# Kernel optimization log

Hardware: AMD Instinct MI355X
Metric: run time of the kernel (lower is better)

Reference implementation:

```python
import jax, jax.numpy as jnp
import numpy as np

HEADS = 8
DIM_HEAD = 64


def setup_inputs() -> dict:
    key = jax.random.key(0)
    ks = jax.random.split(key, 9)
    b, n, d = 2, 2048, 512
    inner = HEADS * DIM_HEAD  # 512
    s = 0.02
    return {
        "x": jax.random.normal(ks[0], (b, n, d), dtype=jnp.float32),
        "attn_bias": jax.random.normal(ks[1], (1, HEADS, n, n), dtype=jnp.float32),
        "Wq": jax.random.normal(ks[2], (d, inner), dtype=jnp.float32) * s,
        "Wkv": jax.random.normal(ks[3], (d, 2 * inner), dtype=jnp.float32) * s,
        "Wo": jax.random.normal(ks[4], (inner, d), dtype=jnp.float32) * s,
        "bo": jax.random.normal(ks[5], (d,), dtype=jnp.float32) * s,
        "Wg": jax.random.normal(ks[6], (d, inner), dtype=jnp.float32) * s,
        "bg": jnp.ones((inner,), dtype=jnp.float32),
    }


def reference(x, attn_bias, Wq, Wkv, Wo, bo, Wg, bg):
    b, n, d = x.shape
    h, dh = HEADS, DIM_HEAD
    scale = dh ** -0.5
    # projections: [b, n, h*dh] -> [b, h, n, dh]
    q = (x @ Wq).reshape(b, n, h, dh).transpose(0, 2, 1, 3) * scale
    k, v = jnp.split(x @ Wkv, 2, axis=-1)
    k = k.reshape(b, n, h, dh).transpose(0, 2, 1, 3)
    v = v.reshape(b, n, h, dh).transpose(0, 2, 1, 3)
    # scores + additive bias; max-subtract softmax (stable, as in original)
    dots = jnp.einsum('bhid,bhjd->bhij', q, k) + attn_bias
    attn = jax.nn.softmax(dots, axis=-1)
    out = jnp.einsum('bhij,bhjd->bhid', attn, v)
    out = out.transpose(0, 2, 1, 3).reshape(b, n, h * dh)
    # gating sigmoid epilogue
    gates = jax.nn.sigmoid(x @ Wg + bg)
    out = out * gates
    return out @ Wo + bo
```

## Files before the change

### kernel.cpp

```cpp
#include <hip/hip_runtime.h>
#include <hip/hip_bf16.h>

typedef __bf16 bf16_t;
typedef __bf16 bf16x8 __attribute__((ext_vector_type(8)));
typedef float f32x4 __attribute__((ext_vector_type(4)));

static __device__ __forceinline__ bf16_t to_bf16(float f) { return (bf16_t)f; }

__global__ void k_convert_x(const float* __restrict__ src, bf16_t* __restrict__ dst, int n8) {
  int i = blockIdx.x * blockDim.x + threadIdx.x;
  if (i >= n8) return;
  const float4* s = reinterpret_cast<const float4*>(src) + (size_t)i * 2;
  float4 a = s[0], b = s[1];
  bf16x8 v;
  v[0]=(bf16_t)a.x; v[1]=(bf16_t)a.y; v[2]=(bf16_t)a.z; v[3]=(bf16_t)a.w;
  v[4]=(bf16_t)b.x; v[5]=(bf16_t)b.y; v[6]=(bf16_t)b.z; v[7]=(bf16_t)b.w;
  reinterpret_cast<bf16x8*>(dst)[i] = v;
}

__global__ void k_transpose_cvt(const float* __restrict__ src, bf16_t* __restrict__ dst, int Nc) {
  __shared__ bf16_t tile[64 * 72];
  const int n0 = blockIdx.x * 64, k0 = blockIdx.y * 64;
  const int t = threadIdx.x;
  #pragma unroll
  for (int it = 0; it < 16; ++it) {
    int c = t + it * 256;
    int kl = c >> 6, nl = c & 63;
    tile[kl * 72 + nl] = to_bf16(src[(size_t)(k0 + kl) * Nc + n0 + nl]);
  }
  __syncthreads();
  #pragma unroll
  for (int it = 0; it < 16; ++it) {
    int c = t + it * 256;
    int nl = c >> 6, kl = c & 63;
    dst[(size_t)(n0 + nl) * 512 + k0 + kl] = tile[kl * 72 + nl];
  }
}

__global__ __launch_bounds__(256) void k_gemm_proj(
    const bf16_t* __restrict__ A,
    const bf16_t* __restrict__ BT,
    const float*  __restrict__ bg,
    bf16_t* __restrict__ qo,
    bf16_t* __restrict__ ko,
    bf16_t* __restrict__ vto,
    float*  __restrict__ go)
{
  __shared__ __align__(16) bf16_t lA[128 * 72];
  __shared__ __align__(16) bf16_t lB[128 * 72];
  const int t = threadIdx.x;
  const int w = t >> 6, lane = t & 63, lr = lane & 15, lg = lane >> 4;
  const int wr = w >> 1, wc = w & 1;
  const int m0 = blockIdx.y * 128, n0 = blockIdx.x * 128;
  f32x4 acc[4][4] = {};
  for (int k0 = 0; k0 < 512; k0 += 64) {
    __syncthreads();
    #pragma unroll
    for (int it = 0; it < 4; ++it) {
      int c = t + it * 256;
      int row = c >> 3, cc = c & 7;
      *reinterpret_cast<bf16x8*>(&lA[row * 72 + cc * 8]) =
          *reinterpret_cast<const bf16x8*>(&A[(size_t)(m0 + row) * 512 + k0 + cc * 8]);
      *reinterpret_cast<bf16x8*>(&lB[row * 72 + cc * 8]) =
          *reinterpret_cast<const bf16x8*>(&BT[(size_t)(n0 + row) * 512 + k0 + cc * 8]);
    }
    __syncthreads();
    #pragma unroll
    for (int kk = 0; kk < 2; ++kk) {
      bf16x8 af[4], bfm[4];
      #pragma unroll
      for (int mf = 0; mf < 4; ++mf)
        af[mf] = *reinterpret_cast<const bf16x8*>(&lA[(wr*64 + mf*16 + lr) * 72 + kk*32 + lg*8]);
      #pragma unroll
      for (int nf = 0; nf < 4; ++nf)
        bfm[nf] = *reinterpret_cast<const bf16x8*>(&lB[(wc*64 + nf*16 + lr) * 72 + kk*32 + lg*8]);
      #pragma unroll
      for (int mf = 0; mf < 4; ++mf)
        #pragma unroll
        for (int nf = 0; nf < 4; ++nf)
          acc[mf][nf] = __builtin_amdgcn_mfma_f32_16x16x32_bf16(af[mf], bfm[nf], acc[mf][nf], 0, 0, 0);
    }
  }
  const int seg = n0 >> 9;
  #pragma unroll
  for (int mf = 0; mf < 4; ++mf) {
    #pragma unroll
    for (int nf = 0; nf < 4; ++nf) {
      #pragma unroll
      for (int r = 0; r < 4; ++r) {
        int rm = m0 + wr*64 + mf*16 + lg*4 + r;
        int cn = n0 + wc*64 + nf*16 + lr;
        float v = acc[mf][nf][r];
        int b = rm >> 11, n = rm & 2047;
        int c = cn & 511;
        if (seg == 0) {
          int h = c >> 6, dh = c & 63;
          qo[((size_t)(b*8 + h) * 2048 + n) * 64 + dh] = to_bf16(v * 0.125f);
        } else if (seg == 1) {
          int h = c >> 6, dh = c & 63;
          ko[((size_t)(b*8 + h) * 2048 + n) * 64 + dh] = to_bf16(v);
        } else if (seg == 2) {
          int h = c >> 6, dh = c & 63;
          vto[((size_t)(b*8 + h) * 64 + dh) * 2048 + n] = to_bf16(v);
        } else {
          float z = v + bg[c];
          go[(size_t)rm * 512 + c] = 1.0f / (1.0f + __expf(-z));
        }
      }
    }
  }
}

#define M_FIX 8.0f
template<int FINAL>
__global__ __launch_bounds__(256, 4) void k_attn(
    const bf16_t* __restrict__ q,
    const bf16_t* __restrict__ kb,
    const bf16_t* __restrict__ vt,
    const float*  __restrict__ bias,
    const float*  __restrict__ gates,
    bf16_t* __restrict__ ao,
    float* __restrict__ pO,
    float* __restrict__ pl)
{
  __shared__ __align__(16) bf16_t lK[64 * 72];
  __shared__ __align__(16) bf16_t lV[64 * 72];
  __shared__ __align__(16) bf16_t lP[4][16 * 72];
  const int t = threadIdx.x, w = t >> 6, lane = t & 63, lr = lane & 15, lg = lane >> 4;
  const int bh = blockIdx.y, b = bh >> 3, h = bh & 7;
  const int i0 = blockIdx.x * 64, ib = i0 + w * 16;
  const int ntile = 32 / (int)gridDim.z;
  const int sz = blockIdx.z;
  const int jbase = sz * ntile * 64;

  bf16x8 aq[2];
  const bf16_t* qp = q + ((size_t)bh * 2048 + ib + lr) * 64;
  aq[0] = *reinterpret_cast<const bf16x8*>(qp + lg * 8);
  aq[1] = *reinterpret_cast<const bf16x8*>(qp + 32 + lg * 8);

  float l_r[4] = {0.f, 0.f, 0.f, 0.f};
  f32x4 accO[4] = {};

  const float* bias_p = bias + (size_t)h * 2048 * 2048 + (size_t)(ib + lg * 4) * 2048 + lr;
  const bf16_t* kp = kb + (size_t)bh * 2048 * 64;
  const bf16_t* vp = vt + (size_t)bh * 64 * 2048;

  const int srow = t >> 3, scc = t & 7;
  const int srow1 = (t + 256) >> 3;

  bf16x8 rK0, rK1, rV0, rV1;
  float bv[4][4];
  {
    const int j0 = jbase;
    rK0 = *reinterpret_cast<const bf16x8*>(&kp[(size_t)(j0 + srow)  * 64 + scc * 8]);
    rK1 = *reinterpret_cast<const bf16x8*>(&kp[(size_t)(j0 + srow1) * 64 + scc * 8]);
    rV0 = *reinterpret_cast<const bf16x8*>(&vp[(size_t)srow  * 2048 + j0 + scc * 8]);
    rV1 = *reinterpret_cast<const bf16x8*>(&vp[(size_t)srow1 * 2048 + j0 + scc * 8]);
    #pragma unroll
    for (int nf = 0; nf < 4; ++nf)
      #pragma unroll
      for (int r = 0; r < 4; ++r)
        bv[nf][r] = bias_p[(size_t)r * 2048 + j0 + nf * 16];
  }

  for (int jt = 0; jt < ntile; ++jt) {
    const int j1 = jbase + (jt + 1) * 64;
    const bool more = (jt + 1 < ntile);

    __syncthreads();
    *reinterpret_cast<bf16x8*>(&lK[srow  * 72 + scc * 8]) = rK0;
    *reinterpret_cast<bf16x8*>(&lK[srow1 * 72 + scc * 8]) = rK1;
    *reinterpret_cast<bf16x8*>(&lV[srow  * 72 + scc * 8]) = rV0;
    *reinterpret_cast<bf16x8*>(&lV[srow1 * 72 + scc * 8]) = rV1;
    __syncthreads();

    if (more) {
      rK0 = *reinterpret_cast<const bf16x8*>(&kp[(size_t)(j1 + srow)  * 64 + scc * 8]);
      rK1 = *reinterpret_cast<const bf16x8*>(&kp[(size_t)(j1 + srow1) * 64 + scc * 8]);
      rV0 = *reinterpret_cast<const bf16x8*>(&vp[(size_t)srow  * 2048 + j1 + scc * 8]);
      rV1 = *reinterpret_cast<const bf16x8*>(&vp[(size_t)srow1 * 2048 + j1 + scc * 8]);
    }

    f32x4 s[4] = {};
    #pragma unroll
    for (int kk = 0; kk < 2; ++kk) {
      #pragma unroll
      for (int nf = 0; nf < 4; ++nf) {
        bf16x8 bf = *reinterpret_cast<const bf16x8*>(&lK[(nf*16 + lr) * 72 + kk*32 + lg*8]);
        s[nf] = __builtin_amdgcn_mfma_f32_16x16x32_bf16(aq[kk], bf, s[nf], 0, 0, 0);
      }
    }
    #pragma unroll
    for (int nf = 0; nf < 4; ++nf) {
      #pragma unroll
      for (int r = 0; r < 4; ++r) {
        float p = __expf(s[nf][r] + bv[nf][r] - M_FIX);
        s[nf][r] = p;
        l_r[r] += p;
        lP[w][(lg*4 + r) * 72 + nf*16 + lr] = to_bf16(p);
      }
    }
    if (more) {
      #pragma unroll
      for (int nf = 0; nf < 4; ++nf)
        #pragma unroll
        for (int r = 0; r < 4; ++r)
          bv[nf][r] = bias_p[(size_t)r * 2048 + j1 + nf * 16];
    }

    #pragma unroll
    for (int kk = 0; kk < 2; ++kk) {
      bf16x8 pa = *reinterpret_cast<const bf16x8*>(&lP[w][lr * 72 + kk*32 + lg*8]);
      #pragma unroll
      for (int df = 0; df < 4; ++df) {
        bf16x8 bv8 = *reinterpret_cast<const bf16x8*>(&lV[(df*16 + lr) * 72 + kk*32 + lg*8]);
        accO[df] = __builtin_amdgcn_mfma_f32_16x16x32_bf16(pa, bv8, accO[df], 0, 0, 0);
      }
    }
  }

  #pragma unroll
  for (int r = 0; r < 4; ++r) {
    float rs = l_r[r];
    rs += __shfl_xor(rs, 1); rs += __shfl_xor(rs, 2);
    rs += __shfl_xor(rs, 4); rs += __shfl_xor(rs, 8);
    l_r[r] = rs;
  }

  if (FINAL) {
    #pragma unroll
    for (int r = 0; r < 4; ++r) {
      float inv = 1.0f / l_r[r];
      int ig = ib + lg*4 + r;
      #pragma unroll
      for (int df = 0; df < 4; ++df) {
        int dg = h*64 + df*16 + lr;
        float gate = gates[(size_t)(b*2048 + ig) * 512 + dg];
        ao[(size_t)(b*2048 + ig) * 512 + dg] = to_bf16(accO[df][r] * inv * gate);
      }
    }
  } else {
    float* po = pO + (((size_t)sz * 16 + bh) * 2048) * 64;
    #pragma unroll
    for (int r = 0; r < 4; ++r) {
      int ig = ib + lg*4 + r;
      #pragma unroll
      for (int df = 0; df < 4; ++df)
        po[(size_t)ig * 64 + df*16 + lr] = accO[df][r];
    }
    if (lr == 0) {
      size_t rb = ((size_t)sz * 16 + bh) * 2048 + ib + lg*4;
      #pragma unroll
      for (int r = 0; r < 4; ++r) pl[rb + r] = l_r[r];
    }
  }
}

__global__ __launch_bounds__(256) void k_attn_combine(
    const float* __restrict__ pO, const float* __restrict__ pl,
    const float* __restrict__ gates, bf16_t* __restrict__ ao, int nsplit)
{
  int idx = blockIdx.x * 256 + threadIdx.x;
  int dh = idx & 63, row = (idx >> 6) & 2047, bh = idx >> 17;
  int b = bh >> 3, h = bh & 7;
  const size_t SP_O = (size_t)16 * 2048 * 64, SP_S = (size_t)16 * 2048;
  size_t rb = (size_t)bh * 2048 + row;
  float L = 0.f, O = 0.f;
  for (int s = 0; s < nsplit; ++s) {
    L += pl[s * SP_S + rb];
    O += pO[s * SP_O + rb * 64 + dh];
  }
  float gate = gates[(size_t)(b * 2048 + row) * 512 + h * 64 + dh];
  ao[(size_t)(b * 2048 + row) * 512 + h * 64 + dh] = to_bf16(O / L * gate);
}

__global__ __launch_bounds__(256) void k_gemm_out(
    const bf16_t* __restrict__ A,
    const bf16_t* __restrict__ BT,
    const float*  __restrict__ bo,
    float* __restrict__ out)
{
  __shared__ __align__(16) bf16_t lA[128 * 72];
  __shared__ __align__(16) bf16_t lB[128 * 72];
  const int t = threadIdx.x;
  const int w = t >> 6, lane = t & 63, lr = lane & 15, lg = lane >> 4;
  const int wr = w >> 1, wc = w & 1;
  const int m0 = blockIdx.y * 128, n0 = blockIdx.x * 128;
  f32x4 acc[4][4] = {};
  for (int k0 = 0; k0 < 512; k0 += 64) {
    __syncthreads();
    #pragma unroll
    for (int it = 0; it < 4; ++it) {
      int c = t + it * 256;
      int row = c >> 3, cc = c & 7;
      *reinterpret_cast<bf16x8*>(&lA[row * 72 + cc * 8]) =
          *reinterpret_cast<const bf16x8*>(&A[(size_t)(m0 + row) * 512 + k0 + cc * 8]);
      *reinterpret_cast<bf16x8*>(&lB[row * 72 + cc * 8]) =
          *reinterpret_cast<const bf16x8*>(&BT[(size_t)(n0 + row) * 512 + k0 + cc * 8]);
    }
    __syncthreads();
    #pragma unroll
    for (int kk = 0; kk < 2; ++kk) {
      bf16x8 af[4], bfm[4];
      #pragma unroll
      for (int mf = 0; mf < 4; ++mf)
        af[mf] = *reinterpret_cast<const bf16x8*>(&lA[(wr*64 + mf*16 + lr) * 72 + kk*32 + lg*8]);
      #pragma unroll
      for (int nf = 0; nf < 4; ++nf)
        bfm[nf] = *reinterpret_cast<const bf16x8*>(&lB[(wc*64 + nf*16 + lr) * 72 + kk*32 + lg*8]);
      #pragma unroll
      for (int mf = 0; mf < 4; ++mf)
        #pragma unroll
        for (int nf = 0; nf < 4; ++nf)
          acc[mf][nf] = __builtin_amdgcn_mfma_f32_16x16x32_bf16(af[mf], bfm[nf], acc[mf][nf], 0, 0, 0);
    }
  }
  #pragma unroll
  for (int mf = 0; mf < 4; ++mf) {
    #pragma unroll
    for (int nf = 0; nf < 4; ++nf) {
      #pragma unroll
      for (int r = 0; r < 4; ++r) {
        int rm = m0 + wr*64 + mf*16 + lg*4 + r;
        int cn = n0 + wc*64 + nf*16 + lr;
        out[(size_t)rm * 512 + cn] = acc[mf][nf][r] + bo[cn];
      }
    }
  }
}

extern "C" void kernel_launch(void* const* d_in, const int* in_sizes, int n_in,
                              void* d_out, int out_size, void* d_ws, size_t ws_size,
                              hipStream_t stream) {
  const float* x    = (const float*)d_in[0];
  const float* bias = (const float*)d_in[1];
  const float* Wq   = (const float*)d_in[2];
  const float* Wkv  = (const float*)d_in[3];
  const float* Wo   = (const float*)d_in[4];
  const float* bo   = (const float*)d_in[5];
  const float* Wg   = (const float*)d_in[6];
  const float* bg   = (const float*)d_in[7];
  float* out = (float*)d_out;

  char* ws = (char*)d_ws;
  const size_t MB = 1024 * 1024;
  bf16_t* x_bf  = (bf16_t*)(ws + 0 * MB);
  bf16_t* WcatT = (bf16_t*)(ws + 4 * MB);
  bf16_t* WoT   = (bf16_t*)(ws + 6 * MB);
  bf16_t* q_bf  = (bf16_t*)(ws + 7 * MB);
  bf16_t* k_bf  = (bf16_t*)(ws + 11 * MB);
  bf16_t* vt_bf = (bf16_t*)(ws + 15 * MB);
  float*  g_f32 = (float*) (ws + 19 * MB);
  bf16_t* ao_bf = (bf16_t*)(ws + 27 * MB);

  int NS = (ws_size >= 66 * MB) ? 4 : (ws_size >= 48 * MB ? 2 : 1);
  float* pO = (float*)(ws + 31 * MB);
  float* pl = (float*)(ws + 31 * MB + (size_t)NS * 8 * MB);

  k_convert_x<<<1024, 256, 0, stream>>>(x, x_bf, 2097152 / 8);
  k_transpose_cvt<<<dim3(8, 8),  256, 0, stream>>>(Wq,  WcatT,               512);
  k_transpose_cvt<<<dim3(16, 8), 256, 0, stream>>>(Wkv, WcatT + 512 * 512,  1024);
  k_transpose_cvt<<<dim3(8, 8),  256, 0, stream>>>(Wg,  WcatT + 1536 * 512,  512);
  k_transpose_cvt<<<dim3(8, 8),  256, 0, stream>>>(Wo,  WoT,                 512);
  k_gemm_proj<<<dim3(16, 32), 256, 0, stream>>>(x_bf, WcatT, bg, q_bf, k_bf, vt_bf, g_f32);

  if (NS > 1) {
    k_attn<0><<<dim3(32, 16, NS), 256, 0, stream>>>(q_bf, k_bf, vt_bf, bias, nullptr,
                                                    nullptr, pO, pl);
    k_attn_combine<<<8192, 256, 0, stream>>>(pO, pl, g_f32, ao_bf, NS);
  } else {
    k_attn<1><<<dim3(32, 16, 1), 256, 0, stream>>>(q_bf, k_bf, vt_bf, bias, g_f32,
                                                   ao_bf, nullptr, nullptr);
  }
  k_gemm_out<<<dim3(4, 32), 256, 0, stream>>>(ao_bf, WoT, bo, out);
}
```

Baseline: 118.3 us.

## Process 32 query rows per wave in attention to reuse K/V tiles

Each wave now handles two 16-row query sub-tiles, so every block covers 128 query rows instead of 64. Each K and V fragment read from shared memory feeds two MFMAs, and each K/V tile staged into LDS is reused by twice as many rows. The grid in the query dimension is halved and the minimum-occupancy hint is dropped. This raises register use and halves the block count, which risks lower occupancy and less latency hiding, particularly for the bias stream.

```diff
diff --git a/kernel.cpp b/kernel.cpp
--- a/kernel.cpp
+++ b/kernel.cpp
@@ -113,7 +113,7 @@
 
 #define M_FIX 8.0f
 template<int FINAL>
-__global__ __launch_bounds__(256, 4) void k_attn(
+__global__ __launch_bounds__(256) void k_attn(
     const bf16_t* __restrict__ q,
     const bf16_t* __restrict__ kb,
     const bf16_t* __restrict__ vt,
@@ -125,21 +125,24 @@
 {
   __shared__ __align__(16) bf16_t lK[64 * 72];
   __shared__ __align__(16) bf16_t lV[64 * 72];
-  __shared__ __align__(16) bf16_t lP[4][16 * 72];
+  __shared__ __align__(16) bf16_t lP[4][32 * 72];
   const int t = threadIdx.x, w = t >> 6, lane = t & 63, lr = lane & 15, lg = lane >> 4;
   const int bh = blockIdx.y, b = bh >> 3, h = bh & 7;
-  const int i0 = blockIdx.x * 64, ib = i0 + w * 16;
+  const int i0 = blockIdx.x * 128, ib = i0 + w * 32;
   const int ntile = 32 / (int)gridDim.z;
   const int sz = blockIdx.z;
   const int jbase = sz * ntile * 64;
 
-  bf16x8 aq[2];
+  bf16x8 aq[2][2];
   const bf16_t* qp = q + ((size_t)bh * 2048 + ib + lr) * 64;
-  aq[0] = *reinterpret_cast<const bf16x8*>(qp + lg * 8);
-  aq[1] = *reinterpret_cast<const bf16x8*>(qp + 32 + lg * 8);
-
-  float l_r[4] = {0.f, 0.f, 0.f, 0.f};
-  f32x4 accO[4] = {};
+  #pragma unroll
+  for (int h2 = 0; h2 < 2; ++h2) {
+    aq[h2][0] = *reinterpret_cast<const bf16x8*>(qp + h2 * 16 * 64 + lg * 8);
+    aq[h2][1] = *reinterpret_cast<const bf16x8*>(qp + h2 * 16 * 64 + 32 + lg * 8);
+  }
+
+  float l_r[2][4] = {};
+  f32x4 accO[2][4] = {};
 
   const float* bias_p = bias + (size_t)h * 2048 * 2048 + (size_t)(ib + lg * 4) * 2048 + lr;
   const bf16_t* kp = kb + (size_t)bh * 2048 * 64;
@@ -149,7 +152,7 @@
   const int srow1 = (t + 256) >> 3;
 
   bf16x8 rK0, rK1, rV0, rV1;
-  float bv[4][4];
+  float bv[2][4][4];
   {
     const int j0 = jbase;
     rK0 = *reinterpret_cast<const bf16x8*>(&kp[(size_t)(j0 + srow)  * 64 + scc * 8]);
@@ -157,10 +160,12 @@
     rV0 = *reinterpret_cast<const bf16x8*>(&vp[(size_t)srow  * 2048 + j0 + scc * 8]);
     rV1 = *reinterpret_cast<const bf16x8*>(&vp[(size_t)srow1 * 2048 + j0 + scc * 8]);
     #pragma unroll
-    for (int nf = 0; nf < 4; ++nf)
-      #pragma unroll
-      for (int r = 0; r < 4; ++r)
-        bv[nf][r] = bias_p[(size_t)r * 2048 + j0 + nf * 16];
+    for (int h2 = 0; h2 < 2; ++h2)
+      #pragma unroll
+      for (int nf = 0; nf < 4; ++nf)
+        #pragma unroll
+        for (int r = 0; r < 4; ++r)
+          bv[h2][nf][r] = bias_p[(size_t)(h2*16 + r) * 2048 + j0 + nf * 16];
   }
 
   for (int jt = 0; jt < ntile; ++jt) {
@@ -181,77 +186,95 @@
       rV1 = *reinterpret_cast<const bf16x8*>(&vp[(size_t)srow1 * 2048 + j1 + scc * 8]);
     }
 
-    f32x4 s[4] = {};
+    f32x4 s[2][4] = {};
     #pragma unroll
     for (int kk = 0; kk < 2; ++kk) {
       #pragma unroll
       for (int nf = 0; nf < 4; ++nf) {
-        bf16x8 bf = *reinterpret_cast<const bf16x8*>(&lK[(nf*16 + lr) * 72 + kk*32 + lg*8]);
-        s[nf] = __builtin_amdgcn_mfma_f32_16x16x32_bf16(aq[kk], bf, s[nf], 0, 0, 0);
-      }
-    }
-    #pragma unroll
-    for (int nf = 0; nf < 4; ++nf) {
+        bf16x8 kf = *reinterpret_cast<const bf16x8*>(&lK[(nf*16 + lr) * 72 + kk*32 + lg*8]);
+        s[0][nf] = __builtin_amdgcn_mfma_f32_16x16x32_bf16(aq[0][kk], kf, s[0][nf], 0, 0, 0);
+        s[1][nf] = __builtin_amdgcn_mfma_f32_16x16x32_bf16(aq[1][kk], kf, s[1][nf], 0, 0, 0);
+      }
+    }
+
+    #pragma unroll
+    for (int h2 = 0; h2 < 2; ++h2) {
+      #pragma unroll
+      for (int nf = 0; nf < 4; ++nf) {
+        #pragma unroll
+        for (int r = 0; r < 4; ++r) {
+          float p = __expf(s[h2][nf][r] + bv[h2][nf][r] - M_FIX);
+          l_r[h2][r] += p;
+          lP[w][(h2*16 + lg*4 + r) * 72 + nf*16 + lr] = to_bf16(p);
+        }
+      }
+    }
+    if (more) {
+      #pragma unroll
+      for (int h2 = 0; h2 < 2; ++h2)
+        #pragma unroll
+        for (int nf = 0; nf < 4; ++nf)
+          #pragma unroll
+          for (int r = 0; r < 4; ++r)
+            bv[h2][nf][r] = bias_p[(size_t)(h2*16 + r) * 2048 + j1 + nf * 16];
+    }
+
+    #pragma unroll
+    for (int kk = 0; kk < 2; ++kk) {
+      bf16x8 pa0 = *reinterpret_cast<const bf16x8*>(&lP[w][(lr)      * 72 + kk*32 + lg*8]);
+      bf16x8 pa1 = *reinterpret_cast<const bf16x8*>(&lP[w][(16 + lr) * 72 + kk*32 + lg*8]);
+      #pragma unroll
+      for (int df = 0; df < 4; ++df) {
+        bf16x8 vb8 = *reinterpret_cast<const bf16x8*>(&lV[(df*16 + lr) * 72 + kk*32 + lg*8]);
+        accO[0][df] = __builtin_amdgcn_mfma_f32_16x16x32_bf16(pa0, vb8, accO[0][df], 0, 0, 0);
+        accO[1][df] = __builtin_amdgcn_mfma_f32_16x16x32_bf16(pa1, vb8, accO[1][df], 0, 0, 0);
+      }
+    }
+  }
+
+  #pragma unroll
+  for (int h2 = 0; h2 < 2; ++h2)
+    #pragma unroll
+    for (int r = 0; r < 4; ++r) {
+      float rs = l_r[h2][r];
+      rs += __shfl_xor(rs, 1); rs += __shfl_xor(rs, 2);
+      rs += __shfl_xor(rs, 4); rs += __shfl_xor(rs, 8);
+      l_r[h2][r] = rs;
+    }
+
+  if (FINAL) {
+    #pragma unroll
+    for (int h2 = 0; h2 < 2; ++h2) {
       #pragma unroll
       for (int r = 0; r < 4; ++r) {
-        float p = __expf(s[nf][r] + bv[nf][r] - M_FIX);
-        s[nf][r] = p;
-        l_r[r] += p;
-        lP[w][(lg*4 + r) * 72 + nf*16 + lr] = to_bf16(p);
-      }
-    }
-    if (more) {
-      #pragma unroll
-      for (int nf = 0; nf < 4; ++nf)
-        #pragma unroll
-        for (int r = 0; r < 4; ++r)
-          bv[nf][r] = bias_p[(size_t)r * 2048 + j1 + nf * 16];
-    }
-
-    #pragma unroll
-    for (int kk = 0; kk < 2; ++kk) {
-      bf16x8 pa = *reinterpret_cast<const bf16x8*>(&lP[w][lr * 72 + kk*32 + lg*8]);
-      #pragma unroll
-      for (int df = 0; df < 4; ++df) {
-        bf16x8 bv8 = *reinterpret_cast<const bf16x8*>(&lV[(df*16 + lr) * 72 + kk*32 + lg*8]);
-        accO[df] = __builtin_amdgcn_mfma_f32_16x16x32_bf16(pa, bv8, accO[df], 0, 0, 0);
-      }
-    }
-  }
-
-  #pragma unroll
-  for (int r = 0; r < 4; ++r) {
-    float rs = l_r[r];
-    rs += __shfl_xor(rs, 1); rs += __shfl_xor(rs, 2);
-    rs += __shfl_xor(rs, 4); rs += __shfl_xor(rs, 8);
-    l_r[r] = rs;
-  }
-
-  if (FINAL) {
-    #pragma unroll
-    for (int r = 0; r < 4; ++r) {
-      float inv = 1.0f / l_r[r];
-      int ig = ib + lg*4 + r;
-      #pragma unroll
-      for (int df = 0; df < 4; ++df) {
-        int dg = h*64 + df*16 + lr;
-        float gate = gates[(size_t)(b*2048 + ig) * 512 + dg];
-        ao[(size_t)(b*2048 + ig) * 512 + dg] = to_bf16(accO[df][r] * inv * gate);
+        float inv = 1.0f / l_r[h2][r];
+        int ig = ib + h2*16 + lg*4 + r;
+        #pragma unroll
+        for (int df = 0; df < 4; ++df) {
+          int dg = h*64 + df*16 + lr;
+          float gate = gates[(size_t)(b*2048 + ig) * 512 + dg];
+          ao[(size_t)(b*2048 + ig) * 512 + dg] = to_bf16(accO[h2][df][r] * inv * gate);
+        }
       }
     }
   } else {
     float* po = pO + (((size_t)sz * 16 + bh) * 2048) * 64;
     #pragma unroll
-    for (int r = 0; r < 4; ++r) {
-      int ig = ib + lg*4 + r;
-      #pragma unroll
-      for (int df = 0; df < 4; ++df)
-        po[(size_t)ig * 64 + df*16 + lr] = accO[df][r];
+    for (int h2 = 0; h2 < 2; ++h2) {
+      #pragma unroll
+      for (int r = 0; r < 4; ++r) {
+        int ig = ib + h2*16 + lg*4 + r;
+        #pragma unroll
+        for (int df = 0; df < 4; ++df)
+          po[(size_t)ig * 64 + df*16 + lr] = accO[h2][df][r];
+      }
     }
     if (lr == 0) {
       size_t rb = ((size_t)sz * 16 + bh) * 2048 + ib + lg*4;
       #pragma unroll
-      for (int r = 0; r < 4; ++r) pl[rb + r] = l_r[r];
+      for (int h2 = 0; h2 < 2; ++h2)
+        #pragma unroll
+        for (int r = 0; r < 4; ++r) pl[rb + h2*16 + r] = l_r[h2][r];
     }
   }
 }
@@ -365,11 +388,11 @@
   k_gemm_proj<<<dim3(16, 32), 256, 0, stream>>>(x_bf, WcatT, bg, q_bf, k_bf, vt_bf, g_f32);
 
   if (NS > 1) {
-    k_attn<0><<<dim3(32, 16, NS), 256, 0, stream>>>(q_bf, k_bf, vt_bf, bias, nullptr,
+    k_attn<0><<<dim3(16, 16, NS), 256, 0, stream>>>(q_bf, k_bf, vt_bf, bias, nullptr,
                                                     nullptr, pO, pl);
     k_attn_combine<<<8192, 256, 0, stream>>>(pO, pl, g_f32, ao_bf, NS);
   } else {
-    k_attn<1><<<dim3(32, 16, 1), 256, 0, stream>>>(q_bf, k_bf, vt_bf, bias, g_f32,
+    k_attn<1><<<dim3(16, 16, 1), 256, 0, stream>>>(q_bf, k_bf, vt_bf, bias, g_f32,
                                                    ao_bf, nullptr, nullptr);
   }
   k_gemm_out<<<dim3(4, 32), 256, 0, stream>>>(ao_bf, WoT, bo, out);
```

Result: faster. 114.2 us (-3.5%).
